# Kernel tuning notes

Measured on AMD Instinct MI355X. Metric: run time of the kernel, lower is better.

Reference implementation:

```python
import jax, jax.numpy as jnp
import numpy as np

B, N, RD = 32, 2000, 32
E, H, A = 128, 256, 8
NUM_ACTIONS = N
ACTION_NORM = float(NUM_ACTIONS)


def _mlp2(x, W1, b1, W2, b2):
    return jnp.maximum(x @ W1 + b1, 0.0) @ W2 + b2


def setup_inputs() -> dict:
    key = jax.random.key(0)
    ks = jax.random.split(key, 8)
    s = lambda fan_in: 1.0 / np.sqrt(fan_in)
    return {
        "state": jax.random.normal(ks[0], (B, N, RD), jnp.float32),
        "distance_matrix": jax.random.uniform(ks[1], (N, N), jnp.float32),
        "W_emb1": jax.random.normal(ks[2], (RD, H), jnp.float32) * s(RD),
        "b_emb1": jnp.zeros((H,), jnp.float32),
        "W_emb2": jax.random.normal(ks[3], (H, E), jnp.float32) * s(H),
        "b_emb2": jnp.zeros((E,), jnp.float32),
        "Wq1": jax.random.normal(ks[4], (E + A, H), jnp.float32) * s(E + A),
        "bq1": jnp.zeros((H,), jnp.float32),
        "Wq2": jax.random.normal(ks[5], (H, 1), jnp.float32) * s(H),
        "bq2": jnp.zeros((1,), jnp.float32),
        "fixed_actions": jax.random.randint(ks[6], (3, B), 0, NUM_ACTIONS, jnp.int32),
        "fixed_agent_ids": jnp.arange(3, dtype=jnp.int32),
    }


def reference(state, distance_matrix, W_emb1, b_emb1, W_emb2, b_emb2,
              Wq1, bq1, Wq2, bq2, fixed_actions, fixed_agent_ids):
    # normalized distance -> similarity, row-stochastic
    dm = distance_matrix / distance_matrix.max()
    sim = jnp.exp(-dm)  # scaling = 1 (use_nn_scaling=False)
    sim = sim / sim.sum(-1, keepdims=True)

    enc = _mlp2(state, W_emb1, b_emb1, W_emb2, b_emb2)      # [B,N,E]
    x = jnp.einsum('nm,bme->bne', sim, enc)                 # graph conv mix

    idx_f = jnp.arange(N, dtype=x.dtype)

    def qnet(actions):
        # actions: [B,A] broadcast over node axis -> concat -> MLP -> [B,N]
        act = jnp.broadcast_to(actions[:, None, :], (B, N, A))
        feat = jnp.concatenate([x, act], axis=-1)           # [B,N,E+A]
        return _mlp2(feat, Wq1, bq1, Wq2, bq2)[..., 0]      # [B,N]

    # init actions: -1 everywhere, fixed agents get given action / norm
    actions = jnp.full((B, A), -1.0, dtype=x.dtype)
    actions = actions.at[:, fixed_agent_ids].set(
        fixed_actions.T.astype(x.dtype) / ACTION_NORM)

    # sequential per-agent soft-argmax loop (second torch loop; the first
    # torch loop's q-values are fully overwritten here, so it is dead code)
    q_cols = []
    for agent_id in range(A):
        q = qnet(actions)                                   # [B,N]
        sam = jnp.clip(jax.nn.softmax(q, axis=-1) @ idx_f, 0.0, float(NUM_ACTIONS))
        actions = actions.at[:, agent_id].set(
            jax.lax.stop_gradient(sam / ACTION_NORM))
        q2 = qnet(actions)
        qv = jnp.take_along_axis(q2, sam.astype(jnp.int32)[:, None], axis=-1)[:, 0]
        q_cols.append(qv)

    q_values = jnp.stack(q_cols, axis=1)                    # [B,A]
    chosen = (actions * ACTION_NORM).astype(jnp.int32)      # [B,A]
    return q_values, chosen
```

## Files before the change

### kernel.cpp

```cpp
#include <hip/hip_runtime.h>
#include <cstddef>

#define NB 32
#define NN 2000
#define NRD 32
#define NE 128
#define NH 256
#define NA 8
#define KP8 2048
#define NGP 128
#define H1S 264
#define XT8S 136
#define ACTION_NORM 2000.0f

typedef unsigned short u16;
typedef unsigned char u8;
typedef __bf16 b16x8 __attribute__((ext_vector_type(8)));
typedef float f32x4 __attribute__((ext_vector_type(4)));
typedef const __attribute__((address_space(1))) unsigned int* gptr_t;
typedef __attribute__((address_space(3))) unsigned int* lptr_t;

__device__ inline u16 f2bf(float x) {
    unsigned u = __float_as_uint(x);
    u += 0x7FFFu + ((u >> 16) & 1u);
    return (u16)(u >> 16);
}
__device__ inline float bf2f(u16 h) { return __uint_as_float((unsigned)h << 16); }
__device__ inline u8 f2fp8(float x) {
    return (u8)(__builtin_amdgcn_cvt_pk_fp8_f32(x, x, 0, false) & 0xFF);
}
__device__ inline u16 f2fp8x2(float a, float b) {
    return (u16)(__builtin_amdgcn_cvt_pk_fp8_f32(a, b, 0, false) & 0xFFFF);
}
__device__ inline float fp82f(u8 b) {
    return __builtin_amdgcn_cvt_pk_f32_fp8((unsigned)b, false)[0];
}
__device__ inline int kswz(int m) {
    return (m & ~63) + (((m >> 3) & 3) << 4) + (((m >> 5) & 1) << 3) + (m & 7);
}

#define PREP_STATE (64000 * 32)
#define PREP_W1T   (256 * 32)
#define PREP_W2T   (128 * 256)
#define PREP_WQ1T  (256 * 128)
#define PREP_PAD   (4096 * 48)
#define PREP_TOT   (PREP_STATE + PREP_W1T + PREP_W2T + PREP_WQ1T + PREP_PAD)
#define PREP_BLOCKS (PREP_TOT / 256)
#define MAX_BLOCKS 1024
__global__ __launch_bounds__(256) void k_front(
        const float* __restrict__ state, const float* __restrict__ W1,
        const float* __restrict__ W2, const float* __restrict__ Wq1,
        const float* __restrict__ dm, const int* __restrict__ fa,
        const int* __restrict__ fid,
        u16* __restrict__ state_b, u16* __restrict__ W1t,
        u16* __restrict__ W2t, u8* __restrict__ Wq1f8,
        u8* __restrict__ encb, float* __restrict__ pmax,
        float* __restrict__ actions, float* __restrict__ ap0,
        float2* __restrict__ part0) {
    __shared__ float sh[256];
    const int blk = blockIdx.x, t = threadIdx.x;
    if (blk < PREP_BLOCKS) {
        int i = blk * 256 + t;
        if (i < PREP_STATE) { state_b[i] = f2bf(state[i]); return; }
        i -= PREP_STATE;
        if (i < PREP_W1T) { int h = i >> 5, k = i & 31; W1t[i] = f2bf(W1[k * NH + h]); return; }
        i -= PREP_W1T;
        if (i < PREP_W2T) { int e = i >> 8, h = i & 255; W2t[i] = f2bf(W2[h * NE + e]); return; }
        i -= PREP_W2T;
        if (i < PREP_WQ1T) { int hq = i >> 7, e = i & 127; Wq1f8[i] = f2fp8(Wq1[e * NH + hq]); return; }
        i -= PREP_WQ1T;
        if (i < PREP_PAD) { int eb = i / 48, mm = NN + (i % 48); encb[(size_t)eb * KP8 + kswz(mm)] = 0; }
        return;
    }
    if (blk < PREP_BLOCKS + MAX_BLOCKS) {
        const int bid = blk - PREP_BLOCKS;
        float m = 0.0f;
        for (size_t i = (size_t)bid * 256 + t; i < (size_t)NN * NN; i += (size_t)MAX_BLOCKS * 256)
            m = fmaxf(m, dm[i]);
        sh[t] = m; __syncthreads();
        for (int s = 128; s > 0; s >>= 1) {
            if (t < s) sh[t] = fmaxf(sh[t], sh[t + s]);
            __syncthreads();
        }
        if (t == 0) pmax[bid] = sh[0];
        return;
    }
    const int b = t >> 3, a = t & 7;
    float v = -1.0f;
    for (int j = 0; j < 3; ++j)
        if (fid[j] == a) v = (float)fa[j * NB + b] / ACTION_NORM;
    actions[t] = v;
    sh[t] = v;
    __syncthreads();
    float wq[NA];
#pragma unroll
    for (int aa = 0; aa < NA; ++aa) wq[aa] = Wq1[(size_t)(NE + aa) * NH + t];
    for (int bb = 0; bb < NB; ++bb) {
        float s = 0.0f;
#pragma unroll
        for (int aa = 0; aa < NA; ++aa) s = fmaf(sh[bb * NA + aa], wq[aa], s);
        ap0[bb * NH + t] = s;
    }
    for (int i = t; i < NB * NGP; i += 256) part0[i] = make_float2(0.0f, 0.0f);
}

__global__ __launch_bounds__(512) void k_sim_enc(
        const u16* __restrict__ state_b, const u16* __restrict__ W1t,
        const u16* __restrict__ W2t, u8* __restrict__ encb,
        const float* __restrict__ b1, const float* __restrict__ b2,
        const float* __restrict__ dm, const float* __restrict__ pmax,
        u8* __restrict__ simb, float* __restrict__ inv_rs) {
    __shared__ u16 stage[20 * 512];
    __shared__ u16 h1t[64 * H1S];
    const int blk = blockIdx.x, tid = threadIdx.x;

    if (blk >= 1000) {
        float* shf = (float*)stage;
        const int n = blk - 1000, t = tid;
        float m = fmaxf(pmax[t], pmax[t + 512]);
        shf[t] = m; __syncthreads();
        for (int s = 256; s > 0; s >>= 1) {
            if (t < s) shf[t] = fmaxf(shf[t], shf[t + s]);
            __syncthreads();
        }
        const float inv = 1.0f / shf[0];
        __syncthreads();
        float s = 0.0f;
        for (int mm = t * 2; mm < KP8; mm += 1024) {
            float e0 = 0.0f, e1 = 0.0f;
            if (mm < NN)     { e0 = expf(-dm[(size_t)n * NN + mm] * inv);     s += e0; }
            if (mm + 1 < NN) { e1 = expf(-dm[(size_t)n * NN + mm + 1] * inv); s += e1; }
            *(u16*)(simb + (size_t)n * KP8 + kswz(mm)) = f2fp8x2(e0, e1);
        }
        shf[t] = s; __syncthreads();
        for (int st = 256; st > 0; st >>= 1) {
            if (t < st) shf[t] += shf[t + st];
            __syncthreads();
        }
        if (t == 0) inv_rs[n] = 1.0f / shf[0];
        return;
    }

    const int w = tid >> 6, l = tid & 63;
    const int lm = l & 15, lq = l >> 4;
    const int gm = blk * 64;

    {
#pragma unroll
        for (int i = 0; i < 3; ++i) {
            const int idx = w * 3 + i;
            if (idx < 20) {
                const u16* gp;
                if (idx < 4) gp = state_b + (size_t)(gm + idx * 16 + lm) * NRD + lq * 8;
                else         gp = W1t + (size_t)((idx - 4) * 16 + lm) * NRD + lq * 8;
                __builtin_amdgcn_global_load_lds((gptr_t)gp, (lptr_t)(stage + idx * 512), 16, 0, 0);
            }
        }
        __syncthreads();
        b16x8 af[4], bf[2];
#pragma unroll
        for (int i = 0; i < 4; ++i) af[i] = *(const b16x8*)(stage + i * 512 + l * 8);
#pragma unroll
        for (int j = 0; j < 2; ++j) bf[j] = *(const b16x8*)(stage + (4 + w * 2 + j) * 512 + l * 8);
        f32x4 acc1[4][2] = {};
#pragma unroll
        for (int i = 0; i < 4; ++i)
#pragma unroll
            for (int j = 0; j < 2; ++j)
                acc1[i][j] = __builtin_amdgcn_mfma_f32_16x16x32_bf16(af[i], bf[j], acc1[i][j], 0, 0, 0);
#pragma unroll
        for (int i = 0; i < 4; ++i)
#pragma unroll
            for (int r = 0; r < 4; ++r) {
                const int row = i * 16 + lq * 4 + r;
#pragma unroll
                for (int j = 0; j < 2; ++j) {
                    const int col = w * 32 + j * 16 + lm;
                    h1t[row * H1S + col] = f2bf(fmaxf(acc1[i][j][r] + b1[col], 0.0f));
                }
            }
    }

    const int wr = w & 3, wc = w >> 2;
    f32x4 acc2[2][2] = {};
    for (int k0 = 0; k0 < NH; k0 += 32) {
        __syncthreads();
        {
            const u16* gp = W2t + (size_t)(w * 16 + lm) * NH + k0 + lq * 8;
            __builtin_amdgcn_global_load_lds((gptr_t)gp, (lptr_t)(stage + w * 512), 16, 0, 0);
        }
        __syncthreads();
        b16x8 af2[2], bf2[2];
#pragma unroll
        for (int i = 0; i < 2; ++i)
            af2[i] = *(const b16x8*)(stage + (wr * 2 + i) * 512 + l * 8);
#pragma unroll
        for (int j = 0; j < 2; ++j)
            bf2[j] = *(const b16x8*)(h1t + (wc * 32 + j * 16 + lm) * H1S + k0 + lq * 8);
#pragma unroll
        for (int i = 0; i < 2; ++i)
#pragma unroll
            for (int j = 0; j < 2; ++j)
                acc2[i][j] = __builtin_amdgcn_mfma_f32_16x16x32_bf16(af2[i], bf2[j], acc2[i][j], 0, 0, 0);
    }
#pragma unroll
    for (int i = 0; i < 2; ++i)
#pragma unroll
        for (int r = 0; r < 4; ++r) {
            const int e = wr * 32 + i * 16 + lq * 4 + r;
            const float bias = b2[e];
#pragma unroll
            for (int j = 0; j < 2; ++j) {
                const int rg = gm + wc * 32 + j * 16 + lm;
                const unsigned bb = (unsigned)rg / 2000u;
                const unsigned mm = (unsigned)rg - bb * 2000u;
                encb[((size_t)bb * 128 + e) * KP8 + kswz((int)mm)] = f2fp8(acc2[i][j][r] + bias);
            }
        }
}

__global__ __launch_bounds__(512) void k_conv_y0(
        const u8* __restrict__ simb, const u8* __restrict__ encb,
        const u8* __restrict__ Wq1f8, const float* __restrict__ inv_rs,
        const float* __restrict__ bq1, const float* __restrict__ ap0,
        const float* __restrict__ Wq2, u8* __restrict__ y0f8,
        float2* __restrict__ part0) {
    __shared__ u8 lds[16 * 1024];
    __shared__ u8 xt8[128 * XT8S];
    __shared__ float qsum[64 * 8];
    const int tid = threadIdx.x;
    const int w = tid >> 6, l = tid & 63;
    const int wr = w & 1, wc = w >> 1;
    const int bm = blockIdx.x * 128;
    const int bb = blockIdx.y;
    const int lm = l & 15, lq = l >> 4;
    const u8* Bt = encb + (size_t)bb * 128 * KP8;

    f32x4 acc[4][2] = {};

    for (int k0 = 0; k0 < KP8; k0 += 64) {
        __syncthreads();
#pragma unroll
        for (int i = 0; i < 2; ++i) {
            const int idx = w * 2 + i;
            const u8* gp;
            if (idx < 8) {
                int row = bm + idx * 16 + lm;
                row = row < NN ? row : NN - 1;
                gp = simb + (size_t)row * KP8 + k0 + lq * 16;
            } else {
                gp = Bt + (size_t)((idx - 8) * 16 + lm) * KP8 + k0 + lq * 16;
            }
            __builtin_amdgcn_global_load_lds((gptr_t)gp, (lptr_t)(lds + idx * 1024), 16, 0, 0);
        }
        __syncthreads();
        const int fo = l * 16;
        typedef long lx2 __attribute__((ext_vector_type(2)));
        lx2 af[4], bf[2];
#pragma unroll
        for (int i = 0; i < 4; ++i)
            af[i] = *(const lx2*)(lds + (wr * 4 + i) * 1024 + fo);
#pragma unroll
        for (int j = 0; j < 2; ++j)
            bf[j] = *(const lx2*)(lds + (8 + wc * 2 + j) * 1024 + fo);
#pragma unroll
        for (int i = 0; i < 4; ++i)
#pragma unroll
            for (int j = 0; j < 2; ++j) {
                acc[i][j] = __builtin_amdgcn_mfma_f32_16x16x32_fp8_fp8(af[i][0], bf[j][0], acc[i][j], 0, 0, 0);
                acc[i][j] = __builtin_amdgcn_mfma_f32_16x16x32_fp8_fp8(af[i][1], bf[j][1], acc[i][j], 0, 0, 0);
            }
    }

    __syncthreads();
#pragma unroll
    for (int i = 0; i < 4; ++i) {
#pragma unroll
        for (int r = 0; r < 4; ++r) {
            const int row = wr * 64 + i * 16 + lq * 4 + r;
            const int gn = bm + row;
            const float rsv = inv_rs[gn < NN ? gn : NN - 1];
#pragma unroll
            for (int j = 0; j < 2; ++j) {
                const int col = wc * 32 + j * 16 + lm;
                xt8[row * XT8S + col] = f2fp8(acc[i][j][r] * rsv);
            }
        }
    }
    __syncthreads();

    const int h0 = w * 32;
    float bq1v[2], apv[2], w2vv[2];
#pragma unroll
    for (int j = 0; j < 2; ++j) {
        const int h = h0 + j * 16 + lm;
        bq1v[j] = bq1[h];
        apv[j] = ap0[bb * NH + h];
        w2vv[j] = Wq2[h];
    }
    float se_tot = 0.0f, sn_tot = 0.0f;

    for (int half = 0; half < 2; ++half) {
        f32x4 acc2[4][2] = {};
#pragma unroll
        for (int ks = 0; ks < 4; ++ks) {
            long bfw[2];
#pragma unroll
            for (int j = 0; j < 2; ++j)
                bfw[j] = *(const long*)(Wq1f8 + (size_t)(h0 + j * 16 + lm) * NE + ks * 32 + lq * 8);
#pragma unroll
            for (int i = 0; i < 4; ++i) {
                const long afx = *(const long*)(xt8 + (half * 64 + i * 16 + lm) * XT8S + ks * 32 + lq * 8);
#pragma unroll
                for (int j = 0; j < 2; ++j)
                    acc2[i][j] = __builtin_amdgcn_mfma_f32_16x16x32_fp8_fp8(afx, bfw[j], acc2[i][j], 0, 0, 0);
            }
        }
#pragma unroll
        for (int i = 0; i < 4; ++i) {
#pragma unroll
            for (int r = 0; r < 4; ++r) {
                const int rl = i * 16 + lq * 4 + r;
                const int n = bm + half * 64 + rl;
                float q = 0.0f;
#pragma unroll
                for (int j = 0; j < 2; ++j) {
                    const float v = acc2[i][j][r] + bq1v[j];
                    if (n < NN) y0f8[((size_t)n * NB + bb) * NH + h0 + j * 16 + lm] = f2fp8(v);
                    q += fmaxf(v + apv[j], 0.0f) * w2vv[j];
                }
#pragma unroll
                for (int off = 1; off < 16; off <<= 1) q += __shfl_xor(q, off);
                if (lm == 0) qsum[rl * 8 + w] = q;
            }
        }
        __syncthreads();
        if (tid < 64) {
            const int n = bm + half * 64 + tid;
            float q = 0.0f;
#pragma unroll
            for (int wv = 0; wv < 8; ++wv) q += qsum[tid * 8 + wv];
            float e = (n < NN) ? expf(fminf(q, 60.0f)) : 0.0f;
            float sne = e * (float)n;
#pragma unroll
            for (int off = 32; off > 0; off >>= 1) {
                e += __shfl_xor(e, off); sne += __shfl_xor(sne, off);
            }
            if (tid == 0) { se_tot += e; sn_tot += sne; }
        }
        __syncthreads();
    }
    if (tid == 0) part0[bb * NGP + blockIdx.x] = make_float2(se_tot, sn_tot);
}

__global__ __launch_bounds__(256) void k_agent(
        const u8* __restrict__ y0f8, const float* __restrict__ Wq1,
        const float* __restrict__ Wq2, const float* __restrict__ bq2,
        float* actions, const float2* __restrict__ pin, float2* __restrict__ pout,
        float* __restrict__ out, int ag) {
    __shared__ float sh[256];
    __shared__ float s_sam;
    const int t = threadIdx.x;
    const int lane = t & 63, wave = t >> 6;
    const int wg = blockIdx.x * 4 + wave;
    const int b = wg & 31, ng = wg >> 5;
    const int hl = lane & 15, qtr = lane >> 4;

    float act[NA];
#pragma unroll
    for (int a = 0; a < NA; ++a) act[a] = actions[b * NA + a];
    {
        const float2 p0 = pin[b * NGP + lane];
        const float2 p1 = pin[b * NGP + 64 + lane];
        float se0 = p0.x + p1.x, sn0 = p0.y + p1.y;
#pragma unroll
        for (int m = 32; m > 0; m >>= 1) {
            se0 += __shfl_xor(se0, m); sn0 += __shfl_xor(sn0, m);
        }
        const float sam = fminf(fmaxf(sn0 / se0, 0.0f), 2000.0f);
        act[ag - 1] = sam * (1.0f / ACTION_NORM);
    }
    float ap16[16] = {};
#pragma unroll
    for (int a = 0; a < NA; ++a) {
        const float av = act[a];
        const float4* wq = (const float4*)(Wq1 + (size_t)(NE + a) * NH + hl * 16);
#pragma unroll
        for (int jj = 0; jj < 4; ++jj) {
            const float4 w4 = wq[jj];
            ap16[jj * 4 + 0] = fmaf(av, w4.x, ap16[jj * 4 + 0]);
            ap16[jj * 4 + 1] = fmaf(av, w4.y, ap16[jj * 4 + 1]);
            ap16[jj * 4 + 2] = fmaf(av, w4.z, ap16[jj * 4 + 2]);
            ap16[jj * 4 + 3] = fmaf(av, w4.w, ap16[jj * 4 + 3]);
        }
    }
    float w2v[16];
    {
        const float4* w2p = (const float4*)(Wq2 + hl * 16);
#pragma unroll
        for (int jj = 0; jj < 4; ++jj) {
            const float4 w4 = w2p[jj];
            w2v[jj * 4 + 0] = w4.x; w2v[jj * 4 + 1] = w4.y;
            w2v[jj * 4 + 2] = w4.z; w2v[jj * 4 + 3] = w4.w;
        }
    }

    float se = 0.0f, sn = 0.0f;
#pragma unroll
    for (int k = 0; k < 4; ++k) {
        const int p = ng + k * NGP;
        if (p >= NN / 4) break;
        const int n = 4 * p + qtr;
        const uint4 yv = *(const uint4*)(y0f8 + (((size_t)n * NB + b) << 8) + hl * 16);
        const unsigned dw[4] = {yv.x, yv.y, yv.z, yv.w};
        float q = 0.0f;
#pragma unroll
        for (int d = 0; d < 4; ++d) {
            const auto lo = __builtin_amdgcn_cvt_pk_f32_fp8(dw[d], false);
            const auto hi = __builtin_amdgcn_cvt_pk_f32_fp8(dw[d], true);
            q += fmaxf(lo[0] + ap16[d * 4 + 0], 0.f) * w2v[d * 4 + 0];
            q += fmaxf(lo[1] + ap16[d * 4 + 1], 0.f) * w2v[d * 4 + 1];
            q += fmaxf(hi[0] + ap16[d * 4 + 2], 0.f) * w2v[d * 4 + 2];
            q += fmaxf(hi[1] + ap16[d * 4 + 3], 0.f) * w2v[d * 4 + 3];
        }
#pragma unroll
        for (int off = 1; off < 16; off <<= 1) q += __shfl_xor(q, off);
        const float e = expf(fminf(q, 60.0f));
        se += e; sn += e * (float)n;
    }
    se += __shfl_xor(se, 16); sn += __shfl_xor(sn, 16);
    se += __shfl_xor(se, 32); sn += __shfl_xor(sn, 32);
    if (lane == 0) pout[b * NGP + ng] = make_float2(se, sn);

    if (blockIdx.x < NB) {
        const int bb = blockIdx.x;
        if (wave == 0) {
            const float2 p0 = pin[bb * NGP + lane];
            const float2 p1 = pin[bb * NGP + 64 + lane];
            float a1 = p0.x + p1.x, a2 = p0.y + p1.y;
#pragma unroll
            for (int m = 32; m > 0; m >>= 1) {
                a1 += __shfl_xor(a1, m); a2 += __shfl_xor(a2, m);
            }
            if (lane == 0) s_sam = fminf(fmaxf(a2 / a1, 0.0f), 2000.0f);
        }
        __syncthreads();
        const float sam = s_sam;
        const float samn = sam * (1.0f / ACTION_NORM);
        float apt = 0.0f;
#pragma unroll
        for (int a = 0; a < NA; ++a) {
            const float av = (a == ag - 1) ? samn : actions[bb * NA + a];
            apt = fmaf(av, Wq1[(size_t)(NE + a) * NH + t], apt);
        }
        int nsel = (int)sam; if (nsel > NN - 1) nsel = NN - 1;
        const float yv = fp82f(y0f8[((size_t)nsel * NB + bb) * NH + t]);
        sh[t] = fmaxf(yv + apt, 0.0f) * Wq2[t];
        __syncthreads();
        for (int s = 128; s > 0; s >>= 1) {
            if (t < s) sh[t] += sh[t + s];
            __syncthreads();
        }
        if (t == 0) {
            out[bb * NA + (ag - 1)] = sh[0] + bq2[0];
            actions[bb * NA + (ag - 1)] = samn;
        }
    }
}

__global__ __launch_bounds__(256) void k_fin(
        const u8* __restrict__ y0f8, const float* __restrict__ Wq1,
        const float* __restrict__ Wq2, const float* __restrict__ bq2,
        const float* __restrict__ actions, const float2* __restrict__ pin,
        float* __restrict__ out) {
    __shared__ float sh[256];
    __shared__ float s_sam;
    const int bb = blockIdx.x, t = threadIdx.x;
    const int lane = t & 63, wave = t >> 6;
    if (wave == 0) {
        const float2 p0 = pin[bb * NGP + lane];
        const float2 p1 = pin[bb * NGP + 64 + lane];
        float a1 = p0.x + p1.x, a2 = p0.y + p1.y;
#pragma unroll
        for (int m = 32; m > 0; m >>= 1) {
            a1 += __shfl_xor(a1, m); a2 += __shfl_xor(a2, m);
        }
        if (lane == 0) s_sam = fminf(fmaxf(a2 / a1, 0.0f), 2000.0f);
    }
    __syncthreads();
    const float sam = s_sam;
    const float samn = sam * (1.0f / ACTION_NORM);
    float apt = 0.0f;
#pragma unroll
    for (int a = 0; a < NA; ++a) {
        const float av = (a == NA - 1) ? samn : actions[bb * NA + a];
        apt = fmaf(av, Wq1[(size_t)(NE + a) * NH + t], apt);
    }
    int nsel = (int)sam; if (nsel > NN - 1) nsel = NN - 1;
    const float yv = fp82f(y0f8[((size_t)nsel * NB + bb) * NH + t]);
    sh[t] = fmaxf(yv + apt, 0.0f) * Wq2[t];
    __syncthreads();
    for (int s = 128; s > 0; s >>= 1) {
        if (t < s) sh[t] += sh[t + s];
        __syncthreads();
    }
    if (t == 0) out[bb * NA + (NA - 1)] = sh[0] + bq2[0];
    if (t < NA) {
        const float av = (t == NA - 1) ? samn : actions[bb * NA + t];
        out[NB * NA + bb * NA + t] = (float)(int)(av * ACTION_NORM);
    }
}

extern "C" void kernel_launch(void* const* d_in, const int* in_sizes, int n_in,
                              void* d_out, int out_size, void* d_ws, size_t ws_size,
                              hipStream_t stream) {
    const float* state = (const float*)d_in[0];
    const float* dm    = (const float*)d_in[1];
    const float* W1    = (const float*)d_in[2];
    const float* b1    = (const float*)d_in[3];
    const float* W2    = (const float*)d_in[4];
    const float* b2    = (const float*)d_in[5];
    const float* Wq1   = (const float*)d_in[6];
    const float* bq1   = (const float*)d_in[7];
    const float* Wq2   = (const float*)d_in[8];
    const float* bq2   = (const float*)d_in[9];
    const int* fa      = (const int*)d_in[10];
    const int* fid     = (const int*)d_in[11];
    float* out = (float*)d_out;

    char* p = (char*)d_ws;
    u8* simb       = (u8*)p;       p += (size_t)NN * KP8;
    u8* encb       = (u8*)p;       p += (size_t)4096 * KP8;
    float* inv_rs  = (float*)p;    p += 2048 * 4;
    float* pmax    = (float*)p;    p += 1024 * 4;
    float* actions = (float*)p;    p += 256 * 4;
    float* ap0     = (float*)p;    p += 8192 * 4;
    float2* part0  = (float2*)p;   p += (size_t)NB * NGP * 8;
    float2* part1  = (float2*)p;   p += (size_t)NB * NGP * 8;
    u16* state_b   = (u16*)p;      p += (size_t)2048000 * 2;
    u16* W1t       = (u16*)p;      p += 8192 * 2;
    u16* W2t       = (u16*)p;      p += 32768 * 2;
    u8* Wq1f8      = (u8*)p;       p += 32768;
    u8* y0f8       = (u8*)p;       p += (size_t)16384000;

    k_front<<<PREP_BLOCKS + MAX_BLOCKS + 1, 256, 0, stream>>>(
        state, W1, W2, Wq1, dm, fa, fid,
        state_b, W1t, W2t, Wq1f8, encb, pmax, actions, ap0, part0);
    k_sim_enc<<<3000, 512, 0, stream>>>(state_b, W1t, W2t, encb, b1, b2,
                                        dm, pmax, simb, inv_rs);
    k_conv_y0<<<dim3(16, 32), 512, 0, stream>>>(simb, encb, Wq1f8, inv_rs, bq1,
                                                ap0, Wq2, y0f8, part0);
    for (int ag = 1; ag < NA; ++ag) {
        const float2* pin  = (ag & 1) ? part0 : part1;
        float2*       pout = (ag & 1) ? part1 : part0;
        k_agent<<<1024, 256, 0, stream>>>(y0f8, Wq1, Wq2, bq2, actions,
                                          pin, pout, out, ag);
    }
    k_fin<<<NB, 256, 0, stream>>>(y0f8, Wq1, Wq2, bq2, actions, part1, out);
}
```

Baseline: 259.1 us.

## Double-buffer LDS staging in encoder second layer and graph-conv GEMM loops

Both the encoder's second-layer GEMM and the fp8 sim×enc graph-conv GEMM now use two LDS buffers. The next K-slice is issued with global_load_lds before the MFMAs run on the current slice, which cuts one barrier per iteration and overlaps global-to-LDS transfer with compute. In exchange, the conv kernel's staging LDS doubles, which may lower occupancy. The encoder path also relies on the existing stage buffer being large enough to hold two slices.

Result: no change. 262.3 us (+1.2%).

```diff
diff --git a/kernel.cpp b/kernel.cpp
--- a/kernel.cpp
+++ b/kernel.cpp
@@ -183,25 +183,31 @@
 
     const int wr = w & 3, wc = w >> 2;
     f32x4 acc2[2][2] = {};
-    for (int k0 = 0; k0 < NH; k0 += 32) {
-        __syncthreads();
-        {
-            const u16* gp = W2t + (size_t)(w * 16 + lm) * NH + k0 + lq * 8;
-            __builtin_amdgcn_global_load_lds((gptr_t)gp, (lptr_t)(stage + w * 512), 16, 0, 0);
-        }
-        __syncthreads();
+    const u16* gpw = W2t + (size_t)(w * 16 + lm) * NH + lq * 8;
+    __syncthreads();
+    __builtin_amdgcn_global_load_lds((gptr_t)gpw, (lptr_t)(stage + w * 512), 16, 0, 0);
+    __syncthreads();
+    for (int t = 0; t < 8; ++t) {
+        const int cur = t & 1;
+        if (t < 7) {
+            gpw += 32;
+            __builtin_amdgcn_global_load_lds((gptr_t)gpw,
+                (lptr_t)(stage + (cur ^ 1) * 4096 + w * 512), 16, 0, 0);
+        }
+        const u16* base = stage + cur * 4096;
         b16x8 af2[2], bf2[2];
 #pragma unroll
         for (int i = 0; i < 2; ++i)
-            af2[i] = *(const b16x8*)(stage + (wr * 2 + i) * 512 + l * 8);
+            af2[i] = *(const b16x8*)(base + (wr * 2 + i) * 512 + l * 8);
 #pragma unroll
         for (int j = 0; j < 2; ++j)
-            bf2[j] = *(const b16x8*)(h1t + (wc * 32 + j * 16 + lm) * H1S + k0 + lq * 8);
+            bf2[j] = *(const b16x8*)(h1t + (wc * 32 + j * 16 + lm) * H1S + t * 32 + lq * 8);
 #pragma unroll
         for (int i = 0; i < 2; ++i)
 #pragma unroll
             for (int j = 0; j < 2; ++j)
                 acc2[i][j] = __builtin_amdgcn_mfma_f32_16x16x32_bf16(af2[i], bf2[j], acc2[i][j], 0, 0, 0);
+        __syncthreads();
     }
 #pragma unroll
     for (int i = 0; i < 2; ++i)
@@ -225,7 +231,7 @@
         const float* __restrict__ bq1, const float* __restrict__ ap0,
         const float* __restrict__ Wq2, u8* __restrict__ y0f8,
         float2* __restrict__ part0) {
-    __shared__ u8 lds[16 * 1024];
+    __shared__ u8 lds[2 * 16 * 1024];
     __shared__ u8 xt8[128 * XT8S];
     __shared__ float qsum[64 * 8];
     const int tid = threadIdx.x;
@@ -235,34 +241,47 @@
     const int bb = blockIdx.y;
     const int lm = l & 15, lq = l >> 4;
     const u8* Bt = encb + (size_t)bb * 128 * KP8;
+    typedef long lx2 __attribute__((ext_vector_type(2)));
 
     f32x4 acc[4][2] = {};
 
-    for (int k0 = 0; k0 < KP8; k0 += 64) {
-        __syncthreads();
-#pragma unroll
-        for (int i = 0; i < 2; ++i) {
-            const int idx = w * 2 + i;
-            const u8* gp;
-            if (idx < 8) {
-                int row = bm + idx * 16 + lm;
-                row = row < NN ? row : NN - 1;
-                gp = simb + (size_t)row * KP8 + k0 + lq * 16;
-            } else {
-                gp = Bt + (size_t)((idx - 8) * 16 + lm) * KP8 + k0 + lq * 16;
-            }
-            __builtin_amdgcn_global_load_lds((gptr_t)gp, (lptr_t)(lds + idx * 1024), 16, 0, 0);
-        }
-        __syncthreads();
+    const u8* gpt[2];
+#pragma unroll
+    for (int i = 0; i < 2; ++i) {
+        const int idx = w * 2 + i;
+        if (idx < 8) {
+            int row = bm + idx * 16 + lm;
+            row = row < NN ? row : NN - 1;
+            gpt[i] = simb + (size_t)row * KP8 + lq * 16;
+        } else {
+            gpt[i] = Bt + (size_t)((idx - 8) * 16 + lm) * KP8 + lq * 16;
+        }
+    }
+#pragma unroll
+    for (int i = 0; i < 2; ++i)
+        __builtin_amdgcn_global_load_lds((gptr_t)gpt[i],
+            (lptr_t)(lds + (w * 2 + i) * 1024), 16, 0, 0);
+    __syncthreads();
+
+    for (int t = 0; t < KP8 / 64; ++t) {
+        const u8* curb = lds + (t & 1) * 16384;
+        if (t < KP8 / 64 - 1) {
+            u8* nxtb = lds + ((t + 1) & 1) * 16384;
+#pragma unroll
+            for (int i = 0; i < 2; ++i) {
+                gpt[i] += 64;
+                __builtin_amdgcn_global_load_lds((gptr_t)gpt[i],
+                    (lptr_t)(nxtb + (w * 2 + i) * 1024), 16, 0, 0);
+            }
+        }
         const int fo = l * 16;
-        typedef long lx2 __attribute__((ext_vector_type(2)));
         lx2 af[4], bf[2];
 #pragma unroll
         for (int i = 0; i < 4; ++i)
-            af[i] = *(const lx2*)(lds + (wr * 4 + i) * 1024 + fo);
+            af[i] = *(const lx2*)(curb + (wr * 4 + i) * 1024 + fo);
 #pragma unroll
         for (int j = 0; j < 2; ++j)
-            bf[j] = *(const lx2*)(lds + (8 + wc * 2 + j) * 1024 + fo);
+            bf[j] = *(const lx2*)(curb + (8 + wc * 2 + j) * 1024 + fo);
 #pragma unroll
         for (int i = 0; i < 4; ++i)
 #pragma unroll
@@ -270,9 +289,9 @@
                 acc[i][j] = __builtin_amdgcn_mfma_f32_16x16x32_fp8_fp8(af[i][0], bf[j][0], acc[i][j], 0, 0, 0);
                 acc[i][j] = __builtin_amdgcn_mfma_f32_16x16x32_fp8_fp8(af[i][1], bf[j][1], acc[i][j], 0, 0, 0);
             }
-    }
-
-    __syncthreads();
+        __syncthreads();
+    }
+
 #pragma unroll
     for (int i = 0; i < 4; ++i) {
 #pragma unroll
```
